# Kernel tuning notes

Hardware: AMD Instinct MI355X
Metric: run time of the kernel (lower is better)

Reference implementation:

```python
import jax, jax.numpy as jnp
import numpy as np

N_USER, N_ITEM, D = 50000, 30000, 64
N = N_USER + N_ITEM
NNZ_UI, NNZ_R, NNZ_II = 1000000, 800000, 300000
IMG_F, TXT_F = 512, 384
EPS = 1e-5


def spmm(rows, cols, vals, x, n_out):
    # sparse [n_out, n_in] @ dense [n_in, d] via gather + segment-sum
    return jax.ops.segment_sum(vals[:, None] * x[cols], rows, num_segments=n_out)


def leaky_relu(x):
    return jnp.where(x >= 0, x, 0.01 * x)


def setup_inputs() -> dict:
    key = jax.random.key(0)
    ks = jax.random.split(key, 32)
    f = lambda i, shape, s=0.05: (jax.random.normal(ks[i], shape, dtype=jnp.float32) * s)
    inp = {
        'user_emb': f(0, (N_USER, D)),
        'item_emb': f(1, (N_ITEM, D)),
        'image_embedding': f(2, (N_ITEM, IMG_F), 1.0),
        'text_embedding': f(3, (N_ITEM, TXT_F), 1.0),
        'W_img': f(4, (IMG_F, D)), 'b_img': jnp.zeros((D,), jnp.float32),
        'bn_g_img': jnp.ones((D,), jnp.float32), 'bn_b_img': jnp.zeros((D,), jnp.float32),
        'W_txt': f(5, (TXT_F, D)), 'b_txt': jnp.zeros((D,), jnp.float32),
        'bn_g_txt': jnp.ones((D,), jnp.float32), 'bn_b_txt': jnp.zeros((D,), jnp.float32),
        'W_gate_img': f(6, (D, D)), 'b_gate_img': jnp.zeros((D,), jnp.float32),
        'W_gate_txt': f(7, (D, D)), 'b_gate_txt': jnp.zeros((D,), jnp.float32),
        'W_common1': f(8, (D, D)), 'b_common1': jnp.zeros((D,), jnp.float32),
        'w_common2': f(9, (D,)),
        'ui_vals': jax.random.uniform(ks[10], (NNZ_UI,), dtype=jnp.float32),
        'R_vals': jax.random.uniform(ks[11], (NNZ_R,), dtype=jnp.float32),
        'ii_img_vals': jax.random.uniform(ks[12], (NNZ_II,), dtype=jnp.float32),
        'ii_txt_vals': jax.random.uniform(ks[13], (NNZ_II,), dtype=jnp.float32),
        'ui_rows': jax.random.randint(ks[14], (NNZ_UI,), 0, N, dtype=jnp.int32),
        'ui_cols': jax.random.randint(ks[15], (NNZ_UI,), 0, N, dtype=jnp.int32),
        'R_rows': jax.random.randint(ks[16], (NNZ_R,), 0, N_USER, dtype=jnp.int32),
        'R_cols': jax.random.randint(ks[17], (NNZ_R,), 0, N_ITEM, dtype=jnp.int32),
        'ii_img_rows': jax.random.randint(ks[18], (NNZ_II,), 0, N_ITEM, dtype=jnp.int32),
        'ii_img_cols': jax.random.randint(ks[19], (NNZ_II,), 0, N_ITEM, dtype=jnp.int32),
        'ii_txt_rows': jax.random.randint(ks[20], (NNZ_II,), 0, N_ITEM, dtype=jnp.int32),
        'ii_txt_cols': jax.random.randint(ks[21], (NNZ_II,), 0, N_ITEM, dtype=jnp.int32),
    }
    return inp


def reference(user_emb, item_emb, image_embedding, text_embedding,
              W_img, b_img, bn_g_img, bn_b_img,
              W_txt, b_txt, bn_g_txt, bn_b_txt,
              W_gate_img, b_gate_img, W_gate_txt, b_gate_txt,
              W_common1, b_common1, w_common2,
              ui_vals, R_vals, ii_img_vals, ii_txt_vals,
              ui_rows, ui_cols, R_rows, R_cols,
              ii_img_rows, ii_img_cols, ii_txt_rows, ii_txt_cols):
    # ---- user_item_GCN: adj = original + diffusion (fused edge list) ----
    cat = jnp.concatenate([item_emb, user_emb], axis=0)  # [N, D], item first per source
    embs = [cat]
    for _ in range(2):
        cat = spmm(ui_rows, ui_cols, ui_vals, cat, N)
        embs.append(cat)
    content_embedding = jnp.stack(embs, axis=1).mean(axis=1)  # [N, D]

    # ---- modal projections (BN inference, dropout=eval identity) ----
    def project(x, W, b, g, beta):
        h = x @ W + b
        h = h * (g / jnp.sqrt(1.0 + EPS)) + beta  # BatchNorm1d, running stats (0, 1)
        return leaky_relu(h)

    img_feat = project(image_embedding, W_img, b_img, bn_g_img, bn_b_img)  # [I, D]
    txt_feat = project(text_embedding, W_txt, b_txt, bn_g_txt, bn_b_txt)

    # ---- item_item_GCN ----
    def modal_branch(feat, Wg, bg, rows, cols, vals):
        it = item_emb * jax.nn.sigmoid(feat @ Wg + bg)  # gated item embedding
        for _ in range(2):
            it = spmm(rows, cols, vals, it, N_ITEM)
        us = spmm(R_rows, R_cols, R_vals, it, N_USER)  # R @ item -> user
        return jnp.concatenate([us, it], axis=0)  # [N, D], user first per source

    image_ui = modal_branch(img_feat, W_gate_img, b_gate_img, ii_img_rows, ii_img_cols, ii_img_vals)
    text_ui = modal_branch(txt_feat, W_gate_txt, b_gate_txt, ii_txt_rows, ii_txt_cols, ii_txt_vals)

    # ---- gate_attention_fusion (non-tiktok: 2 modalities) ----
    def att_score(e):
        return leaky_relu(e @ W_common1 + b_common1) @ w_common2  # [N]

    att = jnp.stack([att_score(image_ui), att_score(text_ui)], axis=-1)  # [N, 2]
    w = jax.nn.softmax(att, axis=-1)
    common = w[:, 0:1] * image_ui + w[:, 1:2] * text_ui
    special_img = image_ui - common
    special_txt = text_ui - common

    return jnp.stack([content_embedding, special_img, special_txt, common], axis=0)  # [4, N, D]
```

## Files before the change

kernel.cpp:

```cpp
#include <hip/hip_runtime.h>

#define N_USER 50000
#define N_ITEM 30000
#define DIM    64
#define NTOT   80000
#define NNZ_UI 1000000
#define NNZ_R  800000
#define NNZ_II 300000
#define IMG_F  512
#define TXT_F  384

#define NROWS_ALL 190000
#define NNZ_ALL   2400000
#define BASE_R    NTOT
#define BASE_II   (NTOT + N_USER)
#define BASE_IT   (NTOT + N_USER + N_ITEM)

#define RB_BITS   9
#define RB_ROWS   512
#define NBUCK     ((NROWS_ALL + RB_ROWS - 1) / RB_ROWS)
#define NBLK_A2   400
#define EDG_A2    6000

#define NBLK_PG   625
#define NBLK_UIP  5000
#define NBLK_I16  1875
#define NBLK_U16  3125
#define NBLK_CP   1875

#define NBLK_M1   (2 * NBLK_PG + NBLK_UIP)
#define NBLK_M2   (NBLK_UIP + 2 * NBLK_I16)
#define NBLK_RC   (NBLK_U16 + 2 * NBLK_CP)

__device__ __forceinline__ int edge_row(int i,
        const int* __restrict__ r0, const int* __restrict__ r1,
        const int* __restrict__ r2, const int* __restrict__ r3){
    if (i < NNZ_UI)                       return r0[i];
    if (i < NNZ_UI + NNZ_R)               return BASE_R  + r1[i - NNZ_UI];
    if (i < NNZ_UI + NNZ_R + NNZ_II)      return BASE_II + r2[i - NNZ_UI - NNZ_R];
    return BASE_IT + r3[i - NNZ_UI - NNZ_R - NNZ_II];
}

__device__ __forceinline__ void edge_all(int i,
        const int* __restrict__ r0, const int* __restrict__ c0, const float* __restrict__ v0,
        const int* __restrict__ r1, const int* __restrict__ c1, const float* __restrict__ v1,
        const int* __restrict__ r2, const int* __restrict__ c2, const float* __restrict__ v2,
        const int* __restrict__ r3, const int* __restrict__ c3, const float* __restrict__ v3,
        int& gr, int& col, float& val){
    if (i < NNZ_UI){
        gr = r0[i]; col = c0[i]; val = v0[i];
    } else if (i < NNZ_UI + NNZ_R){
        int j = i - NNZ_UI;               gr = BASE_R  + r1[j]; col = c1[j]; val = v1[j];
    } else if (i < NNZ_UI + NNZ_R + NNZ_II){
        int j = i - NNZ_UI - NNZ_R;       gr = BASE_II + r2[j]; col = c2[j]; val = v2[j];
    } else {
        int j = i - NNZ_UI - NNZ_R - NNZ_II; gr = BASE_IT + r3[j]; col = c3[j]; val = v3[j];
    }
}

__global__ __launch_bounds__(256) void k_bhist(const int* __restrict__ r0,
        const int* __restrict__ r1, const int* __restrict__ r2,
        const int* __restrict__ r3, int* __restrict__ bcnt){
    __shared__ int h[NBUCK];
    for (int i = threadIdx.x; i < NBUCK; i += 256) h[i] = 0;
    __syncthreads();
    const int stride = gridDim.x * 256;
    for (int i = blockIdx.x * 256 + threadIdx.x; i < NNZ_ALL; i += stride){
        int gr = edge_row(i, r0, r1, r2, r3);
        atomicAdd(&h[gr >> RB_BITS], 1);
    }
    __syncthreads();
    for (int i = threadIdx.x; i < NBUCK; i += 256){
        int c = h[i];
        if (c) atomicAdd(&bcnt[i], c);
    }
}

__global__ __launch_bounds__(512) void k_bscan(const int* __restrict__ bcnt,
        int* __restrict__ bbase, int* __restrict__ off){
    __shared__ int sh[512];
    const int t = threadIdx.x;
    int v = (t < NBUCK) ? bcnt[t] : 0;
    sh[t] = v;
    __syncthreads();
    for (int d = 1; d < 512; d <<= 1){
        int u = (t >= d) ? sh[t - d] : 0;
        __syncthreads();
        sh[t] += u;
        __syncthreads();
    }
    if (t < NBUCK) bbase[t] = sh[t] - v;
    if (t == NBUCK - 1){
        bbase[NBUCK] = sh[t];
        off[NROWS_ALL] = sh[t];
    }
}

__global__ __launch_bounds__(256) void k_bin(
        const int* __restrict__ r0, const int* __restrict__ c0, const float* __restrict__ v0,
        const int* __restrict__ r1, const int* __restrict__ c1, const float* __restrict__ v1,
        const int* __restrict__ r2, const int* __restrict__ c2, const float* __restrict__ v2,
        const int* __restrict__ r3, const int* __restrict__ c3, const float* __restrict__ v3,
        const int* __restrict__ bbase, int* __restrict__ bcur,
        int2* __restrict__ binned){
    __shared__ int lofs[NBUCK];
    __shared__ int lcur[NBUCK];
    const int t = threadIdx.x;
    for (int i = t; i < NBUCK; i += 256){ lofs[i] = 0; lcur[i] = 0; }
    __syncthreads();
    const int s0 = blockIdx.x * EDG_A2, s1 = s0 + EDG_A2;
    for (int i = s0 + t; i < s1; i += 256){
        int gr = edge_row(i, r0, r1, r2, r3);
        atomicAdd(&lofs[gr >> RB_BITS], 1);
    }
    __syncthreads();
    for (int i = t; i < NBUCK; i += 256){
        int c = lofs[i];
        lofs[i] = c ? (bbase[i] + atomicAdd(&bcur[i], c)) : 0;
    }
    __syncthreads();
    for (int i = s0 + t; i < s1; i += 256){
        int gr, col; float val;
        edge_all(i, r0, c0, v0, r1, c1, v1, r2, c2, v2, r3, c3, v3, gr, col, val);
        int b = gr >> RB_BITS;
        int slot = atomicAdd(&lcur[b], 1);
        binned[lofs[b] + slot] = make_int2((col << RB_BITS) | (gr & (RB_ROWS - 1)),
                                           __float_as_int(val));
    }
}

__global__ __launch_bounds__(256) void k_scatter(const int* __restrict__ bbase,
        const int2* __restrict__ binned, int* __restrict__ off,
        int2* __restrict__ csr){
    __shared__ int h[RB_ROWS];
    const int t = threadIdx.x;
    const int b = blockIdx.x;
    const int base = bbase[b];
    const int nb = bbase[b + 1] - base;
    h[t] = 0; h[t + 256] = 0;
    __syncthreads();
    for (int i = t; i < nb; i += 256)
        atomicAdd(&h[binned[base + i].x & (RB_ROWS - 1)], 1);
    __syncthreads();
    if (t < 64){
        int v[8], s = 0;
#pragma unroll
        for (int k = 0; k < 8; ++k){ v[k] = h[t * 8 + k]; s += v[k]; }
        int incl = s;
#pragma unroll
        for (int d = 1; d < 64; d <<= 1){
            int u = __shfl_up(incl, d, 64);
            if (t >= d) incl += u;
        }
        int run = incl - s;
#pragma unroll
        for (int k = 0; k < 8; ++k){ int tmp = v[k]; h[t * 8 + k] = run; run += tmp; }
    }
    __syncthreads();
    const int row0 = b << RB_BITS;
    for (int i = t; i < RB_ROWS; i += 256){
        int r = row0 + i;
        if (r < NROWS_ALL) off[r] = base + h[i];
    }
    __syncthreads();
    for (int i = t; i < nb; i += 256){
        int2 rec = binned[base + i];
        int lr = rec.x & (RB_ROWS - 1);
        int slot = atomicAdd(&h[lr], 1);
        csr[base + slot] = make_int2(rec.x >> RB_BITS, rec.y);
    }
}

__device__ __forceinline__ const float* cat_row(int c,
        const float* __restrict__ item, const float* __restrict__ user){
    return (c < N_ITEM) ? (item + ((long)c << 6)) : (user + ((long)(c - N_ITEM) << 6));
}

__device__ __forceinline__ void pull_body(const int* __restrict__ off,
        const int2* __restrict__ csr, const float* __restrict__ x,
        float* __restrict__ y, int r, int l){
    int s = off[r], e = off[r + 1];
    float4 a0 = {0.f, 0.f, 0.f, 0.f};
    float4 a1 = {0.f, 0.f, 0.f, 0.f};
    int j = s;
    for (; j + 2 <= e; j += 2){
        int2 e0 = csr[j];
        int2 e1 = csr[j + 1];
        float v0 = __int_as_float(e0.y);
        float v1 = __int_as_float(e1.y);
        const float4 x0 = *reinterpret_cast<const float4*>(x + ((long)e0.x << 6) + l);
        const float4 x1 = *reinterpret_cast<const float4*>(x + ((long)e1.x << 6) + l);
        a0.x = fmaf(v0, x0.x, a0.x);
        a0.y = fmaf(v0, x0.y, a0.y);
        a0.z = fmaf(v0, x0.z, a0.z);
        a0.w = fmaf(v0, x0.w, a0.w);
        a1.x = fmaf(v1, x1.x, a1.x);
        a1.y = fmaf(v1, x1.y, a1.y);
        a1.z = fmaf(v1, x1.z, a1.z);
        a1.w = fmaf(v1, x1.w, a1.w);
    }
    if (j < e){
        int2 e0 = csr[j];
        float v0 = __int_as_float(e0.y);
        const float4 x0 = *reinterpret_cast<const float4*>(x + ((long)e0.x << 6) + l);
        a0.x = fmaf(v0, x0.x, a0.x);
        a0.y = fmaf(v0, x0.y, a0.y);
        a0.z = fmaf(v0, x0.z, a0.z);
        a0.w = fmaf(v0, x0.w, a0.w);
    }
    a0.x += a1.x; a0.y += a1.y; a0.z += a1.z; a0.w += a1.w;
    *reinterpret_cast<float4*>(y + ((long)r << 6) + l) = a0;
}

__device__ __forceinline__ void pull_cat_body(const int* __restrict__ off,
        const int2* __restrict__ csr, const float* __restrict__ item,
        const float* __restrict__ user, float* __restrict__ y, int r, int l){
    int s = off[r], e = off[r + 1];
    float4 a0 = {0.f, 0.f, 0.f, 0.f};
    float4 a1 = {0.f, 0.f, 0.f, 0.f};
    int j = s;
    for (; j + 2 <= e; j += 2){
        int2 e0 = csr[j];
        int2 e1 = csr[j + 1];
        float v0 = __int_as_float(e0.y);
        float v1 = __int_as_float(e1.y);
        const float4 x0 = *reinterpret_cast<const float4*>(cat_row(e0.x, item, user) + l);
        const float4 x1 = *reinterpret_cast<const float4*>(cat_row(e1.x, item, user) + l);
        a0.x = fmaf(v0, x0.x, a0.x);
        a0.y = fmaf(v0, x0.y, a0.y);
        a0.z = fmaf(v0, x0.z, a0.z);
        a0.w = fmaf(v0, x0.w, a0.w);
        a1.x = fmaf(v1, x1.x, a1.x);
        a1.y = fmaf(v1, x1.y, a1.y);
        a1.z = fmaf(v1, x1.z, a1.z);
        a1.w = fmaf(v1, x1.w, a1.w);
    }
    if (j < e){
        int2 e0 = csr[j];
        float v0 = __int_as_float(e0.y);
        const float4 x0 = *reinterpret_cast<const float4*>(cat_row(e0.x, item, user) + l);
        a0.x = fmaf(v0, x0.x, a0.x);
        a0.y = fmaf(v0, x0.y, a0.y);
        a0.z = fmaf(v0, x0.z, a0.z);
        a0.w = fmaf(v0, x0.w, a0.w);
    }
    a0.x += a1.x; a0.y += a1.y; a0.z += a1.z; a0.w += a1.w;
    *reinterpret_cast<float4*>(y + ((long)r << 6) + l) = a0;
}

__device__ __forceinline__ void pull_mean_body(const int* __restrict__ off,
        const int2* __restrict__ csr, const float* __restrict__ x,
        const float* __restrict__ item, const float* __restrict__ user,
        float* __restrict__ o0, int r, int l){
    int s = off[r], e = off[r + 1];
    float4 a0 = {0.f, 0.f, 0.f, 0.f};
    float4 a1 = {0.f, 0.f, 0.f, 0.f};
    int j = s;
    for (; j + 2 <= e; j += 2){
        int2 e0 = csr[j];
        int2 e1 = csr[j + 1];
        float v0 = __int_as_float(e0.y);
        float v1 = __int_as_float(e1.y);
        const float4 x0 = *reinterpret_cast<const float4*>(x + ((long)e0.x << 6) + l);
        const float4 x1 = *reinterpret_cast<const float4*>(x + ((long)e1.x << 6) + l);
        a0.x = fmaf(v0, x0.x, a0.x);
        a0.y = fmaf(v0, x0.y, a0.y);
        a0.z = fmaf(v0, x0.z, a0.z);
        a0.w = fmaf(v0, x0.w, a0.w);
        a1.x = fmaf(v1, x1.x, a1.x);
        a1.y = fmaf(v1, x1.y, a1.y);
        a1.z = fmaf(v1, x1.z, a1.z);
        a1.w = fmaf(v1, x1.w, a1.w);
    }
    if (j < e){
        int2 e0 = csr[j];
        float v0 = __int_as_float(e0.y);
        const float4 x0 = *reinterpret_cast<const float4*>(x + ((long)e0.x << 6) + l);
        a0.x = fmaf(v0, x0.x, a0.x);
        a0.y = fmaf(v0, x0.y, a0.y);
        a0.z = fmaf(v0, x0.z, a0.z);
        a0.w = fmaf(v0, x0.w, a0.w);
    }
    const float4 av = *reinterpret_cast<const float4*>(cat_row(r, item, user) + l);
    const float4 xv = *reinterpret_cast<const float4*>(x + ((long)r << 6) + l);
    float4 o;
    o.x = (av.x + xv.x + a0.x + a1.x) * (1.0f / 3.0f);
    o.y = (av.y + xv.y + a0.y + a1.y) * (1.0f / 3.0f);
    o.z = (av.z + xv.z + a0.z + a1.z) * (1.0f / 3.0f);
    o.w = (av.w + xv.w + a0.w + a1.w) * (1.0f / 3.0f);
    *reinterpret_cast<float4*>(o0 + ((long)r << 6) + l) = o;
}

__global__ void k_pull2(const int* __restrict__ offA, const int2* __restrict__ csr,
                        const float* __restrict__ xA, float* __restrict__ yA,
                        const int* __restrict__ offB, const float* __restrict__ xB,
                        float* __restrict__ yB, int nrows, int nblk_half){
    int b = blockIdx.x;
    const int* off; const float* x; float* y;
    if (b < nblk_half){ off = offA; x = xA; y = yA; }
    else              { b -= nblk_half; off = offB; x = xB; y = yB; }
    int t = b * 256 + threadIdx.x;
    int r = t >> 4;
    if (r >= nrows) return;
    pull_body(off, csr, x, y, r, (t & 15) << 2);
}

__global__ __launch_bounds__(256) void k_mega1(
        const int* __restrict__ offUI, const int2* __restrict__ csr,
        const float* __restrict__ user,
        float* __restrict__ hop1out,
        const float* __restrict__ Xi, const float* __restrict__ Wi,
        const float* __restrict__ bi, const float* __restrict__ gi,
        const float* __restrict__ bei, const float* __restrict__ Wgi,
        const float* __restrict__ bgi,
        const float* __restrict__ Xt, const float* __restrict__ Wt,
        const float* __restrict__ bt, const float* __restrict__ gt,
        const float* __restrict__ bet, const float* __restrict__ Wgt,
        const float* __restrict__ bgt,
        const float* __restrict__ item,
        float* __restrict__ Pi, float* __restrict__ Pt){
    __shared__ float xs[48][68];
    __shared__ float ws[64][64];

    if (blockIdx.x >= 2 * NBLK_PG){
        int pb = blockIdx.x - 2 * NBLK_PG;
        int t = pb * 256 + threadIdx.x;
        int r = t >> 4;
        pull_cat_body(offUI, csr, item, user, hop1out, r, (t & 15) << 2);
        return;
    }

    const int t  = threadIdx.x;
    const int tr = t >> 4;
    const int tc = t & 15;
    const int pgb = blockIdx.x;
    const bool isTxt = pgb >= NBLK_PG;
    const int  blk   = isTxt ? (pgb - NBLK_PG) : pgb;
    const int  K     = isTxt ? TXT_F : IMG_F;
    const float* X   = isTxt ? Xt  : Xi;
    const float* W   = isTxt ? Wt  : Wi;
    const float* bb  = isTxt ? bt  : bi;
    const float* gg  = isTxt ? gt  : gi;
    const float* be  = isTxt ? bet : bei;
    const float* Wg  = isTxt ? Wgt : Wgi;
    const float* bg  = isTxt ? bgt : bgi;
    float* outP      = isTxt ? Pt  : Pi;
    const int row0   = blk * 48;

    float acc[3][4];
#pragma unroll
    for (int i = 0; i < 3; ++i)
#pragma unroll
        for (int j = 0; j < 4; ++j) acc[i][j] = 0.f;

    for (int ks = 0; ks < K; ks += 64){
        __syncthreads();
#pragma unroll
        for (int i = 0; i < 3; ++i){
            int r = tr + 16 * i;
            *reinterpret_cast<float4*>(&xs[r][tc * 4]) =
                *reinterpret_cast<const float4*>(X + (long)(row0 + r) * K + ks + tc * 4);
        }
        {
            const float4* wsrc = reinterpret_cast<const float4*>(W + (long)ks * 64);
            float4* wdst = reinterpret_cast<float4*>(&ws[0][0]);
#pragma unroll
            for (int i = 0; i < 4; ++i) wdst[t + 256 * i] = wsrc[t + 256 * i];
        }
        __syncthreads();
#pragma unroll 8
        for (int kk = 0; kk < 64; kk += 2){
            float2 a[3];
#pragma unroll
            for (int i = 0; i < 3; ++i)
                a[i] = *reinterpret_cast<const float2*>(&xs[tr + 16 * i][kk]);
            float4 b0 = *reinterpret_cast<const float4*>(&ws[kk][tc * 4]);
            float4 b1 = *reinterpret_cast<const float4*>(&ws[kk + 1][tc * 4]);
#pragma unroll
            for (int i = 0; i < 3; ++i){
                acc[i][0] = fmaf(a[i].x, b0.x, acc[i][0]);
                acc[i][1] = fmaf(a[i].x, b0.y, acc[i][1]);
                acc[i][2] = fmaf(a[i].x, b0.z, acc[i][2]);
                acc[i][3] = fmaf(a[i].x, b0.w, acc[i][3]);
                acc[i][0] = fmaf(a[i].y, b1.x, acc[i][0]);
                acc[i][1] = fmaf(a[i].y, b1.y, acc[i][1]);
                acc[i][2] = fmaf(a[i].y, b1.z, acc[i][2]);
                acc[i][3] = fmaf(a[i].y, b1.w, acc[i][3]);
            }
        }
    }

    const float4 b4  = reinterpret_cast<const float4*>(bb)[tc];
    const float4 g4  = reinterpret_cast<const float4*>(gg)[tc];
    const float4 be4 = reinterpret_cast<const float4*>(be)[tc];
    __syncthreads();
#pragma unroll
    for (int i = 0; i < 3; ++i){
        int r = tr + 16 * i;
        float4 h;
        h.x = (acc[i][0] + b4.x) * (g4.x * 0.99999500003749943f) + be4.x;
        h.y = (acc[i][1] + b4.y) * (g4.y * 0.99999500003749943f) + be4.y;
        h.z = (acc[i][2] + b4.z) * (g4.z * 0.99999500003749943f) + be4.z;
        h.w = (acc[i][3] + b4.w) * (g4.w * 0.99999500003749943f) + be4.w;
        h.x = (h.x >= 0.f) ? h.x : 0.01f * h.x;
        h.y = (h.y >= 0.f) ? h.y : 0.01f * h.y;
        h.z = (h.z >= 0.f) ? h.z : 0.01f * h.z;
        h.w = (h.w >= 0.f) ? h.w : 0.01f * h.w;
        *reinterpret_cast<float4*>(&xs[r][tc * 4]) = h;
    }
    {
        const float4* wsrc = reinterpret_cast<const float4*>(Wg);
        float4* wdst = reinterpret_cast<float4*>(&ws[0][0]);
#pragma unroll
        for (int i = 0; i < 4; ++i) wdst[t + 256 * i] = wsrc[t + 256 * i];
    }
    __syncthreads();

    float ac2[3][4];
#pragma unroll
    for (int i = 0; i < 3; ++i)
#pragma unroll
        for (int j = 0; j < 4; ++j) ac2[i][j] = 0.f;
#pragma unroll 8
    for (int kk = 0; kk < 64; kk += 2){
        float2 a[3];
#pragma unroll
        for (int i = 0; i < 3; ++i)
            a[i] = *reinterpret_cast<const float2*>(&xs[tr + 16 * i][kk]);
        float4 b0 = *reinterpret_cast<const float4*>(&ws[kk][tc * 4]);
        float4 b1 = *reinterpret_cast<const float4*>(&ws[kk + 1][tc * 4]);
#pragma unroll
        for (int i = 0; i < 3; ++i){
            ac2[i][0] = fmaf(a[i].x, b0.x, ac2[i][0]);
            ac2[i][1] = fmaf(a[i].x, b0.y, ac2[i][1]);
            ac2[i][2] = fmaf(a[i].x, b0.z, ac2[i][2]);
            ac2[i][3] = fmaf(a[i].x, b0.w, ac2[i][3]);
            ac2[i][0] = fmaf(a[i].y, b1.x, ac2[i][0]);
            ac2[i][1] = fmaf(a[i].y, b1.y, ac2[i][1]);
            ac2[i][2] = fmaf(a[i].y, b1.z, ac2[i][2]);
            ac2[i][3] = fmaf(a[i].y, b1.w, ac2[i][3]);
        }
    }

    const float4 bg4 = reinterpret_cast<const float4*>(bg)[tc];
#pragma unroll
    for (int i = 0; i < 3; ++i){
        int r = tr + 16 * i;
        const float4 iv = *reinterpret_cast<const float4*>(
                item + (long)(row0 + r) * 64 + tc * 4);
        float4 o;
        o.x = iv.x / (1.f + __expf(-(ac2[i][0] + bg4.x)));
        o.y = iv.y / (1.f + __expf(-(ac2[i][1] + bg4.y)));
        o.z = iv.z / (1.f + __expf(-(ac2[i][2] + bg4.z)));
        o.w = iv.w / (1.f + __expf(-(ac2[i][3] + bg4.w)));
        *reinterpret_cast<float4*>(outP + (long)(row0 + r) * 64 + tc * 4) = o;
    }
}

__global__ void k_mega2c(const int* __restrict__ offUI, const int2* __restrict__ csr,
        const float* __restrict__ hop1,
        const float* __restrict__ item, const float* __restrict__ user,
        float* __restrict__ o0,
        const int* __restrict__ offI2, const float* __restrict__ P_img,
        float* __restrict__ Q_img,
        const int* __restrict__ offT2, const float* __restrict__ P_txt,
        float* __restrict__ Q_txt){
    const int tid = threadIdx.x;
    if (blockIdx.x < NBLK_UIP){
        int t = blockIdx.x * 256 + tid;
        int r = t >> 4;
        pull_mean_body(offUI, csr, hop1, item, user, o0, r, (t & 15) << 2);
    } else {
        int m = blockIdx.x - NBLK_UIP;
        const int* off; const float* x; float* y;
        if (m < NBLK_I16){ off = offI2; x = P_img; y = Q_img; }
        else             { m -= NBLK_I16; off = offT2; x = P_txt; y = Q_txt; }
        int t = m * 256 + tid;
        int r = t >> 4;
        pull_body(off, csr, x, y, r, (t & 15) << 2);
    }
}

__global__ void k_pullRC(const int* __restrict__ off, const int2* __restrict__ csr,
                         const float* __restrict__ xA, float* __restrict__ yA,
                         const float* __restrict__ xB, float* __restrict__ yB,
                         float* __restrict__ dA, float* __restrict__ dB){
    int bid = blockIdx.x;
    const int tid = threadIdx.x;
    if (bid >= NBLK_U16){
        int c = bid - NBLK_U16;
        const float4* src; float4* dst;
        if (c < NBLK_CP){ src = reinterpret_cast<const float4*>(xA);
                          dst = reinterpret_cast<float4*>(dA); }
        else { c -= NBLK_CP; src = reinterpret_cast<const float4*>(xB);
               dst = reinterpret_cast<float4*>(dB); }
        int i = c * 256 + tid;
        dst[i] = src[i];
        return;
    }
    int t = bid * 256 + tid;
    int r = t >> 4;
    int l = (t & 15) << 2;
    int s = off[r], e = off[r + 1];
    float4 pA0 = {0.f,0.f,0.f,0.f}, pA1 = {0.f,0.f,0.f,0.f};
    float4 pB0 = {0.f,0.f,0.f,0.f}, pB1 = {0.f,0.f,0.f,0.f};
    int j = s;
    for (; j + 2 <= e; j += 2){
        int2 e0 = csr[j];
        int2 e1 = csr[j + 1];
        float v0 = __int_as_float(e0.y);
        float v1 = __int_as_float(e1.y);
        long o0 = ((long)e0.x << 6) + l;
        long o1 = ((long)e1.x << 6) + l;
        const float4 xa0 = *reinterpret_cast<const float4*>(xA + o0);
        const float4 xa1 = *reinterpret_cast<const float4*>(xA + o1);
        const float4 xb0 = *reinterpret_cast<const float4*>(xB + o0);
        const float4 xb1 = *reinterpret_cast<const float4*>(xB + o1);
        pA0.x = fmaf(v0, xa0.x, pA0.x); pA0.y = fmaf(v0, xa0.y, pA0.y);
        pA0.z = fmaf(v0, xa0.z, pA0.z); pA0.w = fmaf(v0, xa0.w, pA0.w);
        pA1.x = fmaf(v1, xa1.x, pA1.x); pA1.y = fmaf(v1, xa1.y, pA1.y);
        pA1.z = fmaf(v1, xa1.z, pA1.z); pA1.w = fmaf(v1, xa1.w, pA1.w);
        pB0.x = fmaf(v0, xb0.x, pB0.x); pB0.y = fmaf(v0, xb0.y, pB0.y);
        pB0.z = fmaf(v0, xb0.z, pB0.z); pB0.w = fmaf(v0, xb0.w, pB0.w);
        pB1.x = fmaf(v1, xb1.x, pB1.x); pB1.y = fmaf(v1, xb1.y, pB1.y);
        pB1.z = fmaf(v1, xb1.z, pB1.z); pB1.w = fmaf(v1, xb1.w, pB1.w);
    }
    if (j < e){
        int2 e0 = csr[j];
        float v0 = __int_as_float(e0.y);
        long o0 = ((long)e0.x << 6) + l;
        const float4 xa0 = *reinterpret_cast<const float4*>(xA + o0);
        const float4 xb0 = *reinterpret_cast<const float4*>(xB + o0);
        pA0.x = fmaf(v0, xa0.x, pA0.x); pA0.y = fmaf(v0, xa0.y, pA0.y);
        pA0.z = fmaf(v0, xa0.z, pA0.z); pA0.w = fmaf(v0, xa0.w, pA0.w);
        pB0.x = fmaf(v0, xb0.x, pB0.x); pB0.y = fmaf(v0, xb0.y, pB0.y);
        pB0.z = fmaf(v0, xb0.z, pB0.z); pB0.w = fmaf(v0, xb0.w, pB0.w);
    }
    pA0.x += pA1.x; pA0.y += pA1.y; pA0.z += pA1.z; pA0.w += pA1.w;
    pB0.x += pB1.x; pB0.y += pB1.y; pB0.z += pB1.z; pB0.w += pB1.w;
    *reinterpret_cast<float4*>(yA + ((long)r << 6) + l) = pA0;
    *reinterpret_cast<float4*>(yB + ((long)r << 6) + l) = pB0;
}

__global__ __launch_bounds__(256) void k_fuse(const float* __restrict__ img,
        const float* __restrict__ txt, const float* __restrict__ W1,
        const float* __restrict__ b1, const float* __restrict__ w2,
        float* __restrict__ out){
    __shared__ float si[64][68];
    __shared__ float st[64][68];
    __shared__ float w1s[64][64];
    const int t  = threadIdx.x;
    const int tr = t >> 4;
    const int tc = t & 15;
    const long row0 = (long)blockIdx.x * 64;

#pragma unroll
    for (int i = 0; i < 4; ++i){
        int r = tr + 16 * i;
        *reinterpret_cast<float4*>(&si[r][tc * 4]) =
            *reinterpret_cast<const float4*>(img + (row0 + r) * 64 + tc * 4);
        *reinterpret_cast<float4*>(&st[r][tc * 4]) =
            *reinterpret_cast<const float4*>(txt + (row0 + r) * 64 + tc * 4);
    }
    {
        const float4* wsrc = reinterpret_cast<const float4*>(W1);
        float4* wdst = reinterpret_cast<float4*>(&w1s[0][0]);
#pragma unroll
        for (int i = 0; i < 4; ++i) wdst[t + 256 * i] = wsrc[t + 256 * i];
    }
    __syncthreads();

    float ai[4][4], at[4][4];
#pragma unroll
    for (int i = 0; i < 4; ++i)
#pragma unroll
        for (int j = 0; j < 4; ++j){ ai[i][j] = 0.f; at[i][j] = 0.f; }

#pragma unroll 8
    for (int kk = 0; kk < 64; kk += 2){
        float4 b0 = *reinterpret_cast<const float4*>(&w1s[kk][tc * 4]);
        float4 b1v = *reinterpret_cast<const float4*>(&w1s[kk + 1][tc * 4]);
#pragma unroll
        for (int i = 0; i < 4; ++i){
            float2 a = *reinterpret_cast<const float2*>(&si[tr + 16 * i][kk]);
            float2 c = *reinterpret_cast<const float2*>(&st[tr + 16 * i][kk]);
            ai[i][0] = fmaf(a.x, b0.x, ai[i][0]);
            ai[i][1] = fmaf(a.x, b0.y, ai[i][1]);
            ai[i][2] = fmaf(a.x, b0.z, ai[i][2]);
            ai[i][3] = fmaf(a.x, b0.w, ai[i][3]);
            ai[i][0] = fmaf(a.y, b1v.x, ai[i][0]);
            ai[i][1] = fmaf(a.y, b1v.y, ai[i][1]);
            ai[i][2] = fmaf(a.y, b1v.z, ai[i][2]);
            ai[i][3] = fmaf(a.y, b1v.w, ai[i][3]);
            at[i][0] = fmaf(c.x, b0.x, at[i][0]);
            at[i][1] = fmaf(c.x, b0.y, at[i][1]);
            at[i][2] = fmaf(c.x, b0.z, at[i][2]);
            at[i][3] = fmaf(c.x, b0.w, at[i][3]);
            at[i][0] = fmaf(c.y, b1v.x, at[i][0]);
            at[i][1] = fmaf(c.y, b1v.y, at[i][1]);
            at[i][2] = fmaf(c.y, b1v.z, at[i][2]);
            at[i][3] = fmaf(c.y, b1v.w, at[i][3]);
        }
    }

    const float4 b14 = reinterpret_cast<const float4*>(b1)[tc];
    const float4 w24 = reinterpret_cast<const float4*>(w2)[tc];
    float pi[4], pt[4];
#pragma unroll
    for (int i = 0; i < 4; ++i){
        float hi0 = ai[i][0] + b14.x; hi0 = (hi0 >= 0.f) ? hi0 : 0.01f * hi0;
        float hi1 = ai[i][1] + b14.y; hi1 = (hi1 >= 0.f) ? hi1 : 0.01f * hi1;
        float hi2 = ai[i][2] + b14.z; hi2 = (hi2 >= 0.f) ? hi2 : 0.01f * hi2;
        float hi3 = ai[i][3] + b14.w; hi3 = (hi3 >= 0.f) ? hi3 : 0.01f * hi3;
        float ht0 = at[i][0] + b14.x; ht0 = (ht0 >= 0.f) ? ht0 : 0.01f * ht0;
        float ht1 = at[i][1] + b14.y; ht1 = (ht1 >= 0.f) ? ht1 : 0.01f * ht1;
        float ht2 = at[i][2] + b14.z; ht2 = (ht2 >= 0.f) ? ht2 : 0.01f * ht2;
        float ht3 = at[i][3] + b14.w; ht3 = (ht3 >= 0.f) ? ht3 : 0.01f * ht3;
        pi[i] = fmaf(hi0, w24.x, fmaf(hi1, w24.y, fmaf(hi2, w24.z, hi3 * w24.w)));
        pt[i] = fmaf(ht0, w24.x, fmaf(ht1, w24.y, fmaf(ht2, w24.z, ht3 * w24.w)));
    }
#pragma unroll
    for (int m = 1; m < 16; m <<= 1){
#pragma unroll
        for (int i = 0; i < 4; ++i){
            pi[i] += __shfl_xor(pi[i], m, 64);
            pt[i] += __shfl_xor(pt[i], m, 64);
        }
    }

    const long NTD = (long)NTOT * DIM;
#pragma unroll
    for (int i = 0; i < 4; ++i){
        int r = tr + 16 * i;
        float mx = fmaxf(pi[i], pt[i]);
        float ei = __expf(pi[i] - mx), et = __expf(pt[i] - mx);
        float inv = 1.f / (ei + et);
        float wi = ei * inv, wt = et * inv;
        const float4 ie = *reinterpret_cast<const float4*>(&si[r][tc * 4]);
        const float4 te = *reinterpret_cast<const float4*>(&st[r][tc * 4]);
        float4 cm, oi, ot;
        cm.x = wi * ie.x + wt * te.x;
        cm.y = wi * ie.y + wt * te.y;
        cm.z = wi * ie.z + wt * te.z;
        cm.w = wi * ie.w + wt * te.w;
        oi.x = ie.x - cm.x; oi.y = ie.y - cm.y; oi.z = ie.z - cm.z; oi.w = ie.w - cm.w;
        ot.x = te.x - cm.x; ot.y = te.y - cm.y; ot.z = te.z - cm.z; ot.w = te.w - cm.w;
        long o = (row0 + r) * 64 + tc * 4;
        *reinterpret_cast<float4*>(out + NTD + o)     = oi;
        *reinterpret_cast<float4*>(out + 2 * NTD + o) = ot;
        *reinterpret_cast<float4*>(out + 3 * NTD + o) = cm;
    }
}

extern "C" void kernel_launch(void* const* d_in, const int* in_sizes, int n_in,
                              void* d_out, int out_size, void* d_ws, size_t ws_size,
                              hipStream_t stream){
    const float* user_emb  = (const float*)d_in[0];
    const float* item_emb  = (const float*)d_in[1];
    const float* image_emb = (const float*)d_in[2];
    const float* text_emb  = (const float*)d_in[3];
    const float* W_img = (const float*)d_in[4];
    const float* b_img = (const float*)d_in[5];
    const float* g_img = (const float*)d_in[6];
    const float* be_img= (const float*)d_in[7];
    const float* W_txt = (const float*)d_in[8];
    const float* b_txt = (const float*)d_in[9];
    const float* g_txt = (const float*)d_in[10];
    const float* be_txt= (const float*)d_in[11];
    const float* W_gi  = (const float*)d_in[12];
    const float* b_gi  = (const float*)d_in[13];
    const float* W_gt  = (const float*)d_in[14];
    const float* b_gt  = (const float*)d_in[15];
    const float* W_c1  = (const float*)d_in[16];
    const float* b_c1  = (const float*)d_in[17];
    const float* w_c2  = (const float*)d_in[18];
    const float* ui_vals = (const float*)d_in[19];
    const float* R_vals  = (const float*)d_in[20];
    const float* ii_iv   = (const float*)d_in[21];
    const float* ii_tv   = (const float*)d_in[22];
    const int* ui_rows = (const int*)d_in[23];
    const int* ui_cols = (const int*)d_in[24];
    const int* R_rows  = (const int*)d_in[25];
    const int* R_cols  = (const int*)d_in[26];
    const int* ii_ir   = (const int*)d_in[27];
    const int* ii_ic   = (const int*)d_in[28];
    const int* ii_tr   = (const int*)d_in[29];
    const int* ii_tc   = (const int*)d_in[30];

    const long ND = (long)NTOT * DIM;
    const long ID = (long)N_ITEM * DIM;
    const long UD = (long)N_USER * DIM;

    float* out = (float*)d_out;
    float* o0 = out;
    float* o1 = out + ND;
    float* o2 = out + 2 * ND;
    float* o3 = out + 3 * ND;

    float* P_img = o3;
    float* P_txt = o3 + ID;
    float* Q_img = o1;
    float* Q_txt = o1 + ID;
    float* H_img = o3;
    float* H_txt = o3 + ID;

    int2* binned = (int2*)o0;

    int2* csr   = (int2*)d_ws;
    int*  off   = (int*)(csr + NNZ_ALL);
    int*  bcnt  = off + NROWS_ALL + 4;
    int*  bcur  = bcnt + NBUCK;
    int*  bbase = bcur + NBUCK;

    hipMemsetAsync(bcnt, 0, 2 * NBUCK * sizeof(int), stream);
    k_bhist<<<512, 256, 0, stream>>>(ui_rows, R_rows, ii_ir, ii_tr, bcnt);
    k_bscan<<<1, 512, 0, stream>>>(bcnt, bbase, off);
    k_bin<<<NBLK_A2, 256, 0, stream>>>(
        ui_rows, ui_cols, ui_vals,  R_rows, R_cols, R_vals,
        ii_ir, ii_ic, ii_iv,        ii_tr, ii_tc, ii_tv,
        bbase, bcur, binned);
    k_scatter<<<NBUCK, 256, 0, stream>>>(bbase, binned, off, csr);

    const int* offUI = off;
    const int* offR  = off + BASE_R;
    const int* offI2 = off + BASE_II;
    const int* offT2 = off + BASE_IT;

    k_mega1<<<NBLK_M1, 256, 0, stream>>>(
        offUI, csr, user_emb, o2,
        image_emb, W_img, b_img, g_img, be_img, W_gi, b_gi,
        text_emb,  W_txt, b_txt, g_txt, be_txt, W_gt, b_gt,
        item_emb, P_img, P_txt);

    k_mega2c<<<NBLK_M2, 256, 0, stream>>>(
        offUI, csr, o2, item_emb, user_emb, o0,
        offI2, P_img, Q_img, offT2, P_txt, Q_txt);

    k_pull2<<<2 * NBLK_I16, 256, 0, stream>>>(
        offI2, csr, Q_img, H_img, offT2, Q_txt, H_txt, N_ITEM, NBLK_I16);

    k_pullRC<<<NBLK_RC, 256, 0, stream>>>(
        offR, csr, H_img, o1, H_txt, o2, o1 + UD, o2 + UD);

    k_fuse<<<NTOT / 64, 256, 0, stream>>>(o1, o2, W_c1, b_c1, w_c2, out);
}
```

Baseline: 561.3 us.

## Unroll SpMM gathers by four and halve projection GEMM shared-memory tile

The CSR pull loops now process four edges per iteration with four independent accumulators, which puts more gather loads in flight to hide memory latency. The projection and gate GEMM in k_mega1 moves from a 64-wide K tile to a 32-wide one, shrinking shared memory from about 29 KB to about 15 KB so more blocks can be resident per CU. The gate GEMM is split into two phases, with the activations held in registers and written to shared memory one half at a time. The costs are more registers in the gather loops, twice as many barriers in the GEMM, and a slightly different summation order.

```diff
diff --git a/kernel.cpp b/kernel.cpp
--- a/kernel.cpp
+++ b/kernel.cpp
@@ -176,39 +176,40 @@
     return (c < N_ITEM) ? (item + ((long)c << 6)) : (user + ((long)(c - N_ITEM) << 6));
 }
 
+__device__ __forceinline__ void fma4(float4& a, float v, const float4& x){
+    a.x = fmaf(v, x.x, a.x);
+    a.y = fmaf(v, x.y, a.y);
+    a.z = fmaf(v, x.z, a.z);
+    a.w = fmaf(v, x.w, a.w);
+}
+
 __device__ __forceinline__ void pull_body(const int* __restrict__ off,
         const int2* __restrict__ csr, const float* __restrict__ x,
         float* __restrict__ y, int r, int l){
     int s = off[r], e = off[r + 1];
-    float4 a0 = {0.f, 0.f, 0.f, 0.f};
-    float4 a1 = {0.f, 0.f, 0.f, 0.f};
+    float4 a0 = {0.f,0.f,0.f,0.f}, a1 = {0.f,0.f,0.f,0.f};
+    float4 a2 = {0.f,0.f,0.f,0.f}, a3 = {0.f,0.f,0.f,0.f};
     int j = s;
-    for (; j + 2 <= e; j += 2){
-        int2 e0 = csr[j];
-        int2 e1 = csr[j + 1];
-        float v0 = __int_as_float(e0.y);
-        float v1 = __int_as_float(e1.y);
+    for (; j + 4 <= e; j += 4){
+        int2 e0 = csr[j], e1 = csr[j+1], e2 = csr[j+2], e3 = csr[j+3];
         const float4 x0 = *reinterpret_cast<const float4*>(x + ((long)e0.x << 6) + l);
         const float4 x1 = *reinterpret_cast<const float4*>(x + ((long)e1.x << 6) + l);
-        a0.x = fmaf(v0, x0.x, a0.x);
-        a0.y = fmaf(v0, x0.y, a0.y);
-        a0.z = fmaf(v0, x0.z, a0.z);
-        a0.w = fmaf(v0, x0.w, a0.w);
-        a1.x = fmaf(v1, x1.x, a1.x);
-        a1.y = fmaf(v1, x1.y, a1.y);
-        a1.z = fmaf(v1, x1.z, a1.z);
-        a1.w = fmaf(v1, x1.w, a1.w);
-    }
-    if (j < e){
+        const float4 x2 = *reinterpret_cast<const float4*>(x + ((long)e2.x << 6) + l);
+        const float4 x3 = *reinterpret_cast<const float4*>(x + ((long)e3.x << 6) + l);
+        fma4(a0, __int_as_float(e0.y), x0);
+        fma4(a1, __int_as_float(e1.y), x1);
+        fma4(a2, __int_as_float(e2.y), x2);
+        fma4(a3, __int_as_float(e3.y), x3);
+    }
+    for (; j < e; ++j){
         int2 e0 = csr[j];
-        float v0 = __int_as_float(e0.y);
         const float4 x0 = *reinterpret_cast<const float4*>(x + ((long)e0.x << 6) + l);
-        a0.x = fmaf(v0, x0.x, a0.x);
-        a0.y = fmaf(v0, x0.y, a0.y);
-        a0.z = fmaf(v0, x0.z, a0.z);
-        a0.w = fmaf(v0, x0.w, a0.w);
-    }
-    a0.x += a1.x; a0.y += a1.y; a0.z += a1.z; a0.w += a1.w;
+        fma4(a0, __int_as_float(e0.y), x0);
+    }
+    a0.x = (a0.x + a1.x) + (a2.x + a3.x);
+    a0.y = (a0.y + a1.y) + (a2.y + a3.y);
+    a0.z = (a0.z + a1.z) + (a2.z + a3.z);
+    a0.w = (a0.w + a1.w) + (a2.w + a3.w);
     *reinterpret_cast<float4*>(y + ((long)r << 6) + l) = a0;
 }
 
@@ -216,35 +217,29 @@
         const int2* __restrict__ csr, const float* __restrict__ item,
         const float* __restrict__ user, float* __restrict__ y, int r, int l){
     int s = off[r], e = off[r + 1];
-    float4 a0 = {0.f, 0.f, 0.f, 0.f};
-    float4 a1 = {0.f, 0.f, 0.f, 0.f};
+    float4 a0 = {0.f,0.f,0.f,0.f}, a1 = {0.f,0.f,0.f,0.f};
+    float4 a2 = {0.f,0.f,0.f,0.f}, a3 = {0.f,0.f,0.f,0.f};
     int j = s;
-    for (; j + 2 <= e; j += 2){
-        int2 e0 = csr[j];
-        int2 e1 = csr[j + 1];
-        float v0 = __int_as_float(e0.y);
-        float v1 = __int_as_float(e1.y);
+    for (; j + 4 <= e; j += 4){
+        int2 e0 = csr[j], e1 = csr[j+1], e2 = csr[j+2], e3 = csr[j+3];
         const float4 x0 = *reinterpret_cast<const float4*>(cat_row(e0.x, item, user) + l);
         const float4 x1 = *reinterpret_cast<const float4*>(cat_row(e1.x, item, user) + l);
-        a0.x = fmaf(v0, x0.x, a0.x);
-        a0.y = fmaf(v0, x0.y, a0.y);
-        a0.z = fmaf(v0, x0.z, a0.z);
-        a0.w = fmaf(v0, x0.w, a0.w);
-        a1.x = fmaf(v1, x1.x, a1.x);
-        a1.y = fmaf(v1, x1.y, a1.y);
-        a1.z = fmaf(v1, x1.z, a1.z);
-        a1.w = fmaf(v1, x1.w, a1.w);
-    }
-    if (j < e){
+        const float4 x2 = *reinterpret_cast<const float4*>(cat_row(e2.x, item, user) + l);
+        const float4 x3 = *reinterpret_cast<const float4*>(cat_row(e3.x, item, user) + l);
+        fma4(a0, __int_as_float(e0.y), x0);
+        fma4(a1, __int_as_float(e1.y), x1);
+        fma4(a2, __int_as_float(e2.y), x2);
+        fma4(a3, __int_as_float(e3.y), x3);
+    }
+    for (; j < e; ++j){
         int2 e0 = csr[j];
-        float v0 = __int_as_float(e0.y);
         const float4 x0 = *reinterpret_cast<const float4*>(cat_row(e0.x, item, user) + l);
-        a0.x = fmaf(v0, x0.x, a0.x);
-        a0.y = fmaf(v0, x0.y, a0.y);
-        a0.z = fmaf(v0, x0.z, a0.z);
-        a0.w = fmaf(v0, x0.w, a0.w);
-    }
-    a0.x += a1.x; a0.y += a1.y; a0.z += a1.z; a0.w += a1.w;
+        fma4(a0, __int_as_float(e0.y), x0);
+    }
+    a0.x = (a0.x + a1.x) + (a2.x + a3.x);
+    a0.y = (a0.y + a1.y) + (a2.y + a3.y);
+    a0.z = (a0.z + a1.z) + (a2.z + a3.z);
+    a0.w = (a0.w + a1.w) + (a2.w + a3.w);
     *reinterpret_cast<float4*>(y + ((long)r << 6) + l) = a0;
 }
 
@@ -253,41 +248,36 @@
         const float* __restrict__ item, const float* __restrict__ user,
         float* __restrict__ o0, int r, int l){
     int s = off[r], e = off[r + 1];
-    float4 a0 = {0.f, 0.f, 0.f, 0.f};
-    float4 a1 = {0.f, 0.f, 0.f, 0.f};
+    float4 a0 = {0.f,0.f,0.f,0.f}, a1 = {0.f,0.f,0.f,0.f};
+    float4 a2 = {0.f,0.f,0.f,0.f}, a3 = {0.f,0.f,0.f,0.f};
     int j = s;
-    for (; j + 2 <= e; j += 2){
-        int2 e0 = csr[j];
-        int2 e1 = csr[j + 1];
-        float v0 = __int_as_float(e0.y);
-        float v1 = __int_as_float(e1.y);
+    for (; j + 4 <= e; j += 4){
+        int2 e0 = csr[j], e1 = csr[j+1], e2 = csr[j+2], e3 = csr[j+3];
         const float4 x0 = *reinterpret_cast<const float4*>(x + ((long)e0.x << 6) + l);
         const float4 x1 = *reinterpret_cast<const float4*>(x + ((long)e1.x << 6) + l);
-        a0.x = fmaf(v0, x0.x, a0.x);
-        a0.y = fmaf(v0, x0.y, a0.y);
-        a0.z = fmaf(v0, x0.z, a0.z);
-        a0.w = fmaf(v0, x0.w, a0.w);
-        a1.x = fmaf(v1, x1.x, a1.x);
-        a1.y = fmaf(v1, x1.y, a1.y);
-        a1.z = fmaf(v1, x1.z, a1.z);
-        a1.w = fmaf(v1, x1.w, a1.w);
-    }
-    if (j < e){
+        const float4 x2 = *reinterpret_cast<const float4*>(x + ((long)e2.x << 6) + l);
+        const float4 x3 = *reinterpret_cast<const float4*>(x + ((long)e3.x << 6) + l);
+        fma4(a0, __int_as_float(e0.y), x0);
+        fma4(a1, __int_as_float(e1.y), x1);
+        fma4(a2, __int_as_float(e2.y), x2);
+        fma4(a3, __int_as_float(e3.y), x3);
+    }
+    for (; j < e; ++j){
         int2 e0 = csr[j];
-        float v0 = __int_as_float(e0.y);
         const float4 x0 = *reinterpret_cast<const float4*>(x + ((long)e0.x << 6) + l);
-        a0.x = fmaf(v0, x0.x, a0.x);
-        a0.y = fmaf(v0, x0.y, a0.y);
-        a0.z = fmaf(v0, x0.z, a0.z);
-        a0.w = fmaf(v0, x0.w, a0.w);
-    }
+        fma4(a0, __int_as_float(e0.y), x0);
+    }
+    a0.x = (a0.x + a1.x) + (a2.x + a3.x);
+    a0.y = (a0.y + a1.y) + (a2.y + a3.y);
+    a0.z = (a0.z + a1.z) + (a2.z + a3.z);
+    a0.w = (a0.w + a1.w) + (a2.w + a3.w);
     const float4 av = *reinterpret_cast<const float4*>(cat_row(r, item, user) + l);
     const float4 xv = *reinterpret_cast<const float4*>(x + ((long)r << 6) + l);
     float4 o;
-    o.x = (av.x + xv.x + a0.x + a1.x) * (1.0f / 3.0f);
-    o.y = (av.y + xv.y + a0.y + a1.y) * (1.0f / 3.0f);
-    o.z = (av.z + xv.z + a0.z + a1.z) * (1.0f / 3.0f);
-    o.w = (av.w + xv.w + a0.w + a1.w) * (1.0f / 3.0f);
+    o.x = (av.x + xv.x + a0.x) * (1.0f / 3.0f);
+    o.y = (av.y + xv.y + a0.y) * (1.0f / 3.0f);
+    o.z = (av.z + xv.z + a0.z) * (1.0f / 3.0f);
+    o.w = (av.w + xv.w + a0.w) * (1.0f / 3.0f);
     *reinterpret_cast<float4*>(o0 + ((long)r << 6) + l) = o;
 }
 
@@ -319,8 +309,8 @@
         const float* __restrict__ bgt,
         const float* __restrict__ item,
         float* __restrict__ Pi, float* __restrict__ Pt){
-    __shared__ float xs[48][68];
-    __shared__ float ws[64][64];
+    __shared__ float xs[48][36];
+    __shared__ float ws[32][64];
 
     if (blockIdx.x >= 2 * NBLK_PG){
         int pb = blockIdx.x - 2 * NBLK_PG;
@@ -353,23 +343,28 @@
 #pragma unroll
         for (int j = 0; j < 4; ++j) acc[i][j] = 0.f;
 
-    for (int ks = 0; ks < K; ks += 64){
+    for (int ks = 0; ks < K; ks += 32){
         __syncthreads();
-#pragma unroll
-        for (int i = 0; i < 3; ++i){
-            int r = tr + 16 * i;
-            *reinterpret_cast<float4*>(&xs[r][tc * 4]) =
-                *reinterpret_cast<const float4*>(X + (long)(row0 + r) * K + ks + tc * 4);
+        {
+            int row = t >> 3, col = (t & 7) << 2;
+            *reinterpret_cast<float4*>(&xs[row][col]) =
+                *reinterpret_cast<const float4*>(X + (long)(row0 + row) * K + ks + col);
+            int f = t + 256;
+            if (f < 384){
+                row = f >> 3; col = (f & 7) << 2;
+                *reinterpret_cast<float4*>(&xs[row][col]) =
+                    *reinterpret_cast<const float4*>(X + (long)(row0 + row) * K + ks + col);
+            }
         }
         {
             const float4* wsrc = reinterpret_cast<const float4*>(W + (long)ks * 64);
             float4* wdst = reinterpret_cast<float4*>(&ws[0][0]);
-#pragma unroll
-            for (int i = 0; i < 4; ++i) wdst[t + 256 * i] = wsrc[t + 256 * i];
+            wdst[t]       = wsrc[t];
+            wdst[t + 256] = wsrc[t + 256];
         }
         __syncthreads();
 #pragma unroll 8
-        for (int kk = 0; kk < 64; kk += 2){
+        for (int kk = 0; kk < 32; kk += 2){
             float2 a[3];
 #pragma unroll
             for (int i = 0; i < 3; ++i)
@@ -393,52 +388,60 @@
     const float4 b4  = reinterpret_cast<const float4*>(bb)[tc];
     const float4 g4  = reinterpret_cast<const float4*>(gg)[tc];
     const float4 be4 = reinterpret_cast<const float4*>(be)[tc];
-    __syncthreads();
+    float4 h[3];
 #pragma unroll
     for (int i = 0; i < 3; ++i){
-        int r = tr + 16 * i;
-        float4 h;
-        h.x = (acc[i][0] + b4.x) * (g4.x * 0.99999500003749943f) + be4.x;
-        h.y = (acc[i][1] + b4.y) * (g4.y * 0.99999500003749943f) + be4.y;
-        h.z = (acc[i][2] + b4.z) * (g4.z * 0.99999500003749943f) + be4.z;
-        h.w = (acc[i][3] + b4.w) * (g4.w * 0.99999500003749943f) + be4.w;
-        h.x = (h.x >= 0.f) ? h.x : 0.01f * h.x;
-        h.y = (h.y >= 0.f) ? h.y : 0.01f * h.y;
-        h.z = (h.z >= 0.f) ? h.z : 0.01f * h.z;
-        h.w = (h.w >= 0.f) ? h.w : 0.01f * h.w;
-        *reinterpret_cast<float4*>(&xs[r][tc * 4]) = h;
-    }
-    {
-        const float4* wsrc = reinterpret_cast<const float4*>(Wg);
-        float4* wdst = reinterpret_cast<float4*>(&ws[0][0]);
-#pragma unroll
-        for (int i = 0; i < 4; ++i) wdst[t + 256 * i] = wsrc[t + 256 * i];
-    }
-    __syncthreads();
+        h[i].x = (acc[i][0] + b4.x) * (g4.x * 0.99999500003749943f) + be4.x;
+        h[i].y = (acc[i][1] + b4.y) * (g4.y * 0.99999500003749943f) + be4.y;
+        h[i].z = (acc[i][2] + b4.z) * (g4.z * 0.99999500003749943f) + be4.z;
+        h[i].w = (acc[i][3] + b4.w) * (g4.w * 0.99999500003749943f) + be4.w;
+        h[i].x = (h[i].x >= 0.f) ? h[i].x : 0.01f * h[i].x;
+        h[i].y = (h[i].y >= 0.f) ? h[i].y : 0.01f * h[i].y;
+        h[i].z = (h[i].z >= 0.f) ? h[i].z : 0.01f * h[i].z;
+        h[i].w = (h[i].w >= 0.f) ? h[i].w : 0.01f * h[i].w;
+    }
 
     float ac2[3][4];
 #pragma unroll
     for (int i = 0; i < 3; ++i)
 #pragma unroll
         for (int j = 0; j < 4; ++j) ac2[i][j] = 0.f;
+
+#pragma unroll
+    for (int ph = 0; ph < 2; ++ph){
+        __syncthreads();
+        if ((tc >> 3) == ph){
+            int lc = (tc & 7) << 2;
+#pragma unroll
+            for (int i = 0; i < 3; ++i)
+                *reinterpret_cast<float4*>(&xs[tr + 16 * i][lc]) = h[i];
+        }
+        {
+            const float4* wsrc = reinterpret_cast<const float4*>(Wg) + ph * 512;
+            float4* wdst = reinterpret_cast<float4*>(&ws[0][0]);
+            wdst[t]       = wsrc[t];
+            wdst[t + 256] = wsrc[t + 256];
+        }
+        __syncthreads();
 #pragma unroll 8
-    for (int kk = 0; kk < 64; kk += 2){
-        float2 a[3];
-#pragma unroll
-        for (int i = 0; i < 3; ++i)
-            a[i] = *reinterpret_cast<const float2*>(&xs[tr + 16 * i][kk]);
-        float4 b0 = *reinterpret_cast<const float4*>(&ws[kk][tc * 4]);
-        float4 b1 = *reinterpret_cast<const float4*>(&ws[kk + 1][tc * 4]);
-#pragma unroll
-        for (int i = 0; i < 3; ++i){
-            ac2[i][0] = fmaf(a[i].x, b0.x, ac2[i][0]);
-            ac2[i][1] = fmaf(a[i].x, b0.y, ac2[i][1]);
-            ac2[i][2] = fmaf(a[i].x, b0.z, ac2[i][2]);
-            ac2[i][3] = fmaf(a[i].x, b0.w, ac2[i][3]);
-            ac2[i][0] = fmaf(a[i].y, b1.x, ac2[i][0]);
-            ac2[i][1] = fmaf(a[i].y, b1.y, ac2[i][1]);
-            ac2[i][2] = fmaf(a[i].y, b1.z, ac2[i][2]);
-            ac2[i][3] = fmaf(a[i].y, b1.w, ac2[i][3]);
+        for (int kk = 0; kk < 32; kk += 2){
+            float2 a[3];
+#pragma unroll
+            for (int i = 0; i < 3; ++i)
+                a[i] = *reinterpret_cast<const float2*>(&xs[tr + 16 * i][kk]);
+            float4 b0 = *reinterpret_cast<const float4*>(&ws[kk][tc * 4]);
+            float4 b1 = *reinterpret_cast<const float4*>(&ws[kk + 1][tc * 4]);
+#pragma unroll
+            for (int i = 0; i < 3; ++i){
+                ac2[i][0] = fmaf(a[i].x, b0.x, ac2[i][0]);
+                ac2[i][1] = fmaf(a[i].x, b0.y, ac2[i][1]);
+                ac2[i][2] = fmaf(a[i].x, b0.z, ac2[i][2]);
+                ac2[i][3] = fmaf(a[i].x, b0.w, ac2[i][3]);
+                ac2[i][0] = fmaf(a[i].y, b1.x, ac2[i][0]);
+                ac2[i][1] = fmaf(a[i].y, b1.y, ac2[i][1]);
+                ac2[i][2] = fmaf(a[i].y, b1.z, ac2[i][2]);
+                ac2[i][3] = fmaf(a[i].y, b1.w, ac2[i][3]);
+            }
         }
     }
 
@@ -516,14 +519,10 @@
         const float4 xa1 = *reinterpret_cast<const float4*>(xA + o1);
         const float4 xb0 = *reinterpret_cast<const float4*>(xB + o0);
         const float4 xb1 = *reinterpret_cast<const float4*>(xB + o1);
-        pA0.x = fmaf(v0, xa0.x, pA0.x); pA0.y = fmaf(v0, xa0.y, pA0.y);
-        pA0.z = fmaf(v0, xa0.z, pA0.z); pA0.w = fmaf(v0, xa0.w, pA0.w);
-        pA1.x = fmaf(v1, xa1.x, pA1.x); pA1.y = fmaf(v1, xa1.y, pA1.y);
-        pA1.z = fmaf(v1, xa1.z, pA1.z); pA1.w = fmaf(v1, xa1.w, pA1.w);
-        pB0.x = fmaf(v0, xb0.x, pB0.x); pB0.y = fmaf(v0, xb0.y, pB0.y);
-        pB0.z = fmaf(v0, xb0.z, pB0.z); pB0.w = fmaf(v0, xb0.w, pB0.w);
-        pB1.x = fmaf(v1, xb1.x, pB1.x); pB1.y = fmaf(v1, xb1.y, pB1.y);
-        pB1.z = fmaf(v1, xb1.z, pB1.z); pB1.w = fmaf(v1, xb1.w, pB1.w);
+        fma4(pA0, v0, xa0);
+        fma4(pA1, v1, xa1);
+        fma4(pB0, v0, xb0);
+        fma4(pB1, v1, xb1);
     }
     if (j < e){
         int2 e0 = csr[j];
@@ -531,10 +530,8 @@
         long o0 = ((long)e0.x << 6) + l;
         const float4 xa0 = *reinterpret_cast<const float4*>(xA + o0);
         const float4 xb0 = *reinterpret_cast<const float4*>(xB + o0);
-        pA0.x = fmaf(v0, xa0.x, pA0.x); pA0.y = fmaf(v0, xa0.y, pA0.y);
-        pA0.z = fmaf(v0, xa0.z, pA0.z); pA0.w = fmaf(v0, xa0.w, pA0.w);
-        pB0.x = fmaf(v0, xb0.x, pB0.x); pB0.y = fmaf(v0, xb0.y, pB0.y);
-        pB0.z = fmaf(v0, xb0.z, pB0.z); pB0.w = fmaf(v0, xb0.w, pB0.w);
+        fma4(pA0, v0, xa0);
+        fma4(pB0, v0, xb0);
     }
     pA0.x += pA1.x; pA0.y += pA1.y; pA0.z += pA1.z; pA0.w += pA1.w;
     pB0.x += pB1.x; pB0.y += pB1.y; pB0.z += pB1.z; pB0.w += pB1.w;
```

New measurement: 562.5 us. About the same (+0.2%).
